# Kernel optimization log

Hardware: AMD Instinct MI355X
Metric: run time of the kernel (lower is better)

## Reference

```python
import jax, jax.numpy as jnp
import numpy as np

SEQ_LEN = 1024
D_MODEL = 512
K_FILT = 24
HEADS = 8
R = 512  # must equal d_model for the module's forward to type-check
NFFT = 2048  # nearest power of two >= 2*SEQ_LEN-1
LN_EPS = 1e-5


def _spectral_filters():
    # Hankel matrix Z[i,j] = 2 / ((i+j)^3 - (i+j)), i,j in 1..T
    e = np.arange(1, SEQ_LEN + 1, dtype=np.float64)
    ipj = e[:, None] + e[None, :]
    Z = 2.0 / (ipj ** 3 - ipj)
    sigma, phi = np.linalg.eigh(Z)
    sigma_k = np.clip(sigma[-K_FILT:], 1e-9, None)
    phi_k = phi[:, -K_FILT:] * sigma_k ** 0.25
    return phi_k.astype(np.float32)  # (T, K)


def setup_inputs() -> dict:
    key = jax.random.key(0)
    ks = jax.random.split(key, 12)
    s = 0.02
    B = 2

    def lin(k):
        kw, kb = jax.random.split(k)
        return (jax.random.normal(kw, (D_MODEL, D_MODEL), jnp.float32) * s,
                jax.random.normal(kb, (D_MODEL,), jnp.float32) * s)

    Wq, bq = lin(ks[0]); Wk, bk = lin(ks[1]); Wv, bv = lin(ks[2])
    Wg, bg = lin(ks[3]); Wo, bo = lin(ks[4])
    return {
        'x': jax.random.normal(ks[5], (B, SEQ_LEN, D_MODEL), jnp.float32),
        'stu_filters': jnp.asarray(_spectral_filters()),
        'M_inputs': jax.random.normal(ks[6], (D_MODEL, R), jnp.float32) * s,
        'M_filters': jax.random.normal(ks[7], (K_FILT, R), jnp.float32) * s,
        'Wq': Wq, 'bq': bq, 'Wk': Wk, 'bk': bk, 'Wv': Wv, 'bv': bv,
        'Wg': Wg, 'bg': bg, 'Wo': Wo, 'bo': bo,
        'ln_w': jnp.ones((R,), jnp.float32),
        'ln_b': jnp.zeros((R,), jnp.float32),
    }


def _stu_conv(u, v):
    # u: (B, T, r), v: (T, r). FFT-based causal conv with sign featurization.
    T = u.shape[1]
    sgn = jnp.where(jnp.arange(T) % 2 == 1, -1.0, 1.0)[None, :, None]  # (1,T,1)
    Vf = jnp.fft.rfft(v[None, :, :, None], n=NFFT, axis=1)  # (1,F,r,1)
    U = jnp.stack([u, u * sgn], axis=-1)  # (B,T,r,2)
    Uf = jnp.fft.rfft(U, n=NFFT, axis=1)  # (B,F,r,2)
    conv = jnp.fft.irfft(Vf * Uf, n=NFFT, axis=1)[:, :T]  # (B,T,r,2)
    return conv[..., 0], conv[..., 1] * sgn


def _layernorm(x, w, b):
    mu = jnp.mean(x, axis=-1, keepdims=True)
    var = jnp.mean((x - mu) ** 2, axis=-1, keepdims=True)
    return (x - mu) * jax.lax.rsqrt(var + LN_EPS) * w + b


def reference(x, stu_filters, M_inputs, M_filters, Wq, bq, Wk, bk, Wv, bv,
              Wg, bg, Wo, bo, ln_w, ln_b):
    B, T, d = x.shape
    hd = d // HEADS
    # STU features
    u_proj = x @ M_inputs                    # (B,T,r)
    phi_proj = stu_filters @ M_filters       # (T,r)
    sp, sm = _stu_conv(u_proj, phi_proj)
    x_tilde = _layernorm(sp + sm, ln_w, ln_b)  # (B,T,r==d)
    # gated linear attention with gelu features and causal cumsum state
    def proj(W, b):
        y = (x @ W.T + b).reshape(B, T, HEADS, hd).transpose(0, 2, 1, 3)
        return jax.nn.gelu(y, approximate=True)
    Q = proj(Wq, bq); K = proj(Wk, bk); V = proj(Wv, bv)
    Zt = jnp.einsum('bhtp,bhtn->bhtpn', V, K)   # (B,H,T,hd,hd)
    Hc = jnp.cumsum(Zt, axis=2)
    Y = jnp.einsum('bhtp,bhtpn->bhtn', Q, Hc)   # (B,H,T,hd)
    Y_attn = Y.transpose(0, 2, 1, 3).reshape(B, T, d)
    gate = jax.nn.sigmoid(x @ Wg.T + bg)
    comb = gate * Y_attn + (1.0 - gate) * x_tilde
    return comb @ Wo.T + bo
```

## Files before the change

### kernel.cpp

```cpp
#include <hip/hip_runtime.h>
#include <hip/hip_bf16.h>

#define T_SEQ 1024
#define D_MOD 512
#define NHEAD 8
#define HDIM  64
#define R_DIM 512
#define BATCH 2

typedef __attribute__((ext_vector_type(8))) __bf16 bf16x8;
typedef __attribute__((ext_vector_type(4))) __bf16 bf16x4;
typedef __attribute__((ext_vector_type(4))) float f32x4;

__device__ __forceinline__ float ldin(const void* p, size_t i, int bf) {
    if (bf) return __bfloat162float(((const __hip_bfloat16*)p)[i]);
    return ((const float*)p)[i];
}
__device__ __forceinline__ void stout(void* p, size_t i, int bf, float v) {
    if (bf) ((__hip_bfloat16*)p)[i] = __float2bfloat16(v);
    else    ((float*)p)[i] = v;
}

__device__ __forceinline__ float gelu_f(float x) {
    return 0.5f * x * (1.f + tanhf(0.7978845608028654f * (x + 0.044715f * x * x * x)));
}

__device__ __forceinline__ bf16x8 cvt8(float4 a, float4 b) {
    bf16x8 t;
    t[0]=(__bf16)a.x; t[1]=(__bf16)a.y; t[2]=(__bf16)a.z; t[3]=(__bf16)a.w;
    t[4]=(__bf16)b.x; t[5]=(__bf16)b.y; t[6]=(__bf16)b.z; t[7]=(__bf16)b.w;
    return t;
}

template<int BF>
__global__ __launch_bounds__(256) void mega_gemm(
    const void* __restrict__ x, const void* __restrict__ Mi,
    const void* __restrict__ stf, const void* __restrict__ Mf,
    const void* __restrict__ Wq, const void* __restrict__ bq,
    const void* __restrict__ Wk, const void* __restrict__ bk,
    const void* __restrict__ Wv, const void* __restrict__ bv,
    const void* __restrict__ Wg, const void* __restrict__ bg,
    __bf16* __restrict__ fu, __bf16* __restrict__ fphi,
    __bf16* __restrict__ fQ, __bf16* __restrict__ fKT,
    __bf16* __restrict__ fV, __bf16* __restrict__ fG)
{
    const int tid = threadIdx.x;
    const int job = blockIdx.z;
    if (job == 6) {
        float4* zp = (float4*)(fphi + 524288);
        const int bid = blockIdx.y * 8 + blockIdx.x;
        const float4 z4 = make_float4(0.f, 0.f, 0.f, 0.f);
        #pragma unroll
        for (int q = 0; q < 8; ++q)
            zp[(size_t)bid * 2048 + q * 256 + tid] = z4;
        return;
    }
    constexpr int bf = BF;
    const void* A = x; const void* Bw; const void* bias = nullptr;
    int Kd = 512, act = 0; bool trb = true;
    switch (job) {
        case 0: Bw = Mi; trb = false; break;
        case 1: Bw = Wq; bias = bq; act = 1; break;
        case 2: Bw = Wk; bias = bk; act = 1; break;
        case 3: Bw = Wv; bias = bv; act = 1; break;
        case 4: Bw = Wg; bias = bg; act = 2; break;
        default: A = stf; Bw = Mf; trb = false; Kd = 32; break;
    }
    const int M = (job == 5) ? 1024 : 2048;
    const int m0 = blockIdx.y * 64;
    if (m0 >= M) return;
    const int n0 = blockIdx.x * 64;

    __shared__ __align__(16) __bf16 As[64][40];
    __shared__ __align__(16) __bf16 Bs[64][40];
    const int wave = tid >> 6, lane = tid & 63;
    const int lm = lane & 15, kq = lane >> 4;

    f32x4 acc[4] = {};

    for (int k0 = 0; k0 < Kd; k0 += 32) {
        if (k0) __syncthreads();
        {
            const int mo = tid >> 2;
            const int ko = (tid & 3) * 8;
            if (job == 5) {
                bf16x8 t;
                #pragma unroll
                for (int q = 0; q < 8; ++q) {
                    const int k = ko + q;
                    t[q] = (k < 24) ? (__bf16)ldin(A, (size_t)(m0 + mo) * 24 + k, bf)
                                    : (__bf16)0.f;
                }
                *(bf16x8*)&As[mo][ko] = t;
            } else if (bf) {
                *(bf16x8*)&As[mo][ko] =
                    *(const bf16x8*)((const __bf16*)A + (size_t)(m0 + mo) * 512 + k0 + ko);
            } else {
                const float* Af = (const float*)A + (size_t)(m0 + mo) * 512 + k0 + ko;
                *(bf16x8*)&As[mo][ko] = cvt8(*(const float4*)Af, *(const float4*)(Af + 4));
            }
        }
        if (trb) {
            const int no = tid >> 2;
            const int ko = (tid & 3) * 8;
            const int cs = ((((ko >> 3) ^ (no >> 3)) & 3) << 3);
            const size_t go = (size_t)(n0 + no) * 512 + k0 + ko;
            if (bf) {
                *(bf16x8*)&Bs[no][cs] = *(const bf16x8*)((const __bf16*)Bw + go);
            } else {
                const float* Bf = (const float*)Bw + go;
                *(bf16x8*)&Bs[no][cs] = cvt8(*(const float4*)Bf, *(const float4*)(Bf + 4));
            }
        } else {
            const int kk = tid >> 3;
            const int nn = (tid & 7) * 8;
            if (job == 5) {
                #pragma unroll
                for (int q = 0; q < 8; ++q) {
                    const int row = nn + q;
                    const int c = ((((kk >> 3) ^ (row >> 3)) & 3) << 3) | (kk & 7);
                    Bs[row][c] = (kk < 24) ? (__bf16)ldin(Bw, (size_t)kk * 512 + n0 + row, bf)
                                           : (__bf16)0.f;
                }
            } else {
                const size_t off = (size_t)(k0 + kk) * 512 + n0 + nn;
                bf16x8 t;
                if (bf) {
                    t = *(const bf16x8*)((const __bf16*)Bw + off);
                } else {
                    const float* Bf = (const float*)Bw + off;
                    t = cvt8(*(const float4*)Bf, *(const float4*)(Bf + 4));
                }
                #pragma unroll
                for (int q = 0; q < 8; ++q) {
                    const int row = nn + q;
                    const int c = ((((kk >> 3) ^ (row >> 3)) & 3) << 3) | (kk & 7);
                    Bs[row][c] = t[q];
                }
            }
        }
        __syncthreads();
        const bf16x8 a = *(const bf16x8*)&As[wave * 16 + lm][kq * 8];
        #pragma unroll
        for (int nt = 0; nt < 4; ++nt) {
            const int row = nt * 16 + lm;
            const bf16x8 b = *(const bf16x8*)&Bs[row][(((kq ^ (row >> 3)) & 3) << 3)];
            acc[nt] = __builtin_amdgcn_mfma_f32_16x16x32_bf16(a, b, acc[nt], 0, 0, 0);
        }
    }
    #pragma unroll
    for (int nt = 0; nt < 4; ++nt) {
        const int n = n0 + nt * 16 + lm;
        #pragma unroll
        for (int r2 = 0; r2 < 4; ++r2) {
            const int m = m0 + wave * 16 + kq * 4 + r2;
            float v = acc[nt][r2];
            if (bias) v += ldin(bias, (size_t)n, bf);
            if (act == 1) v = gelu_f(v);
            if (act == 2) v = 1.f / (1.f + expf(-v));
            switch (job) {
                case 0: fu[(size_t)m * 512 + n] = (__bf16)v; break;
                case 5: fphi[(size_t)m * 512 + n] = (__bf16)v; break;
                case 1: fQ[(size_t)m * 512 + n] = (__bf16)v; break;
                case 3: fV[(size_t)m * 512 + n] = (__bf16)v; break;
                case 4: fG[(size_t)m * 512 + n] = (__bf16)v; break;
                case 2: {
                    const int b = m >> 10, t = m & 1023;
                    const int h = n >> 6,  p = n & 63;
                    fKT[(((size_t)b * NHEAD + h) * 64 + p) * T_SEQ + t] = (__bf16)v;
                    break;
                }
            }
        }
    }
}

__global__ __launch_bounds__(256) void conv_attn_k(
    const __bf16* __restrict__ u, const __bf16* __restrict__ vphi,
    float* __restrict__ w,
    const __bf16* __restrict__ Q, const __bf16* __restrict__ KT,
    const __bf16* __restrict__ V, float* __restrict__ Y)
{
    __shared__ __align__(16) unsigned char smem[49152];
    const int tid = threadIdx.x;
    const int z = blockIdx.z;
    int rem = blockIdx.x, ti = 0;
    while (rem >= ((ti + 4) >> 2)) { rem -= (ti + 4) >> 2; ++ti; }
    const int jlo = rem * 4;
    const int jhi = (jlo + 3 < ti) ? jlo + 3 : ti;
    const int t0 = ti * 64;

    if (z < 2) {
        float (*vs)[64] = (float (*)[64])smem;
        float (*us)[64] = (float (*)[64])(smem + 16384);
        const int rl = tid & 63, tg = tid >> 6;
        const int b = z;
        const int r0 = blockIdx.y * 64;
        const __bf16* ub = u + (size_t)b * T_SEQ * R_DIM;
        float acc[16] = {};
        for (int j = jlo; j <= jhi; ++j) {
            if (j != jlo) __syncthreads();
            const int L0 = j * 64;
            const int W0 = t0 - L0 - 63;
            #pragma unroll
            for (int jj = 0; jj < 8; ++jj) {
                const int n = jj * 256 + tid;
                const int row = n >> 4, c4 = (n & 15) * 4;
                int s = W0 + row;
                s = s < 0 ? 0 : (s > T_SEQ - 1 ? T_SEQ - 1 : s);
                const bf16x4 t = *(const bf16x4*)&ub[(size_t)s * R_DIM + r0 + c4];
                *(float4*)&us[row][c4] =
                    make_float4((float)t[0], (float)t[1], (float)t[2], (float)t[3]);
            }
            #pragma unroll
            for (int jj = 0; jj < 4; ++jj) {
                const int n = jj * 256 + tid;
                const int row = n >> 4, c4 = (n & 15) * 4;
                const bf16x4 t = *(const bf16x4*)&vphi[(size_t)(L0 + row) * R_DIM + r0 + c4];
                *(float4*)&vs[row][c4] =
                    make_float4((float)t[0], (float)t[1], (float)t[2], (float)t[3]);
            }
            __syncthreads();
            if (j < ti) {
                #pragma unroll
                for (int g = 0; g < 4; ++g) {
                    const int wsmin = tg * 16 + 49 - 16 * g;
                    float ur[30];
                    #pragma unroll
                    for (int q = 0; q < 30; ++q) ur[q] = us[wsmin + q][rl];
                    float vr[8];
                    #pragma unroll
                    for (int e = 0; e < 8; ++e) vr[e] = vs[16 * g + 2 * e][rl];
                    #pragma unroll
                    for (int e = 0; e < 8; ++e)
                        #pragma unroll
                        for (int i = 0; i < 16; ++i)
                            acc[i] += vr[e] * ur[i - 2 * e + 14];
                }
            } else {
                for (int l = 0; l < 64; l += 2) {
                    const float vv = vs[l][rl];
                    #pragma unroll
                    for (int i = 0; i < 16; ++i) {
                        const int srel = tg * 16 + i - l;
                        if (srel >= 0) acc[i] += vv * us[srel + 63][rl];
                    }
                }
            }
        }
        #pragma unroll
        for (int i = 0; i < 16; ++i)
            atomicAdd(&w[((size_t)b * T_SEQ + t0 + tg * 16 + i) * R_DIM + r0 + rl],
                      2.f * acc[i]);
    } else {
        __bf16 (*Qs)[72] = (__bf16 (*)[72])smem;
        __bf16 (*Vs)[72] = (__bf16 (*)[72])(smem + 9216);
        __bf16 (*Kt)[72] = (__bf16 (*)[72])(smem + 18432);
        __bf16 (*Sa)[72] = (__bf16 (*)[72])(smem + 27648);
        const int wave = tid >> 6, lane = tid & 63;
        const int lm = lane & 15, kq = lane >> 4;
        const int b = z - 2;
        const int h = blockIdx.y;
        const size_t cbase = ((size_t)b * T_SEQ) * D_MOD + h * HDIM;
        const __bf16* KTh = KT + (((size_t)b * NHEAD + h) * 64) * T_SEQ;
        #pragma unroll
        for (int it = 0; it < 2; ++it) {
            const int n = it * 256 + tid;
            const int row = n >> 3, p0 = (n & 7) * 8;
            *(bf16x8*)&Qs[row][p0] = *(const bf16x8*)&Q[cbase + (size_t)(t0 + row) * D_MOD + p0];
        }
        f32x4 accY[4] = {};
        for (int j = jlo; j <= jhi; ++j) {
            const int s0 = j * 64;
            __syncthreads();
            #pragma unroll
            for (int it = 0; it < 2; ++it) {
                const int n = it * 256 + tid;
                const int row = n >> 3, c0 = (n & 7) * 8;
                *(bf16x8*)&Vs[row][c0] = *(const bf16x8*)&V[cbase + (size_t)(s0 + row) * D_MOD + c0];
                *(bf16x8*)&Kt[row][c0] = *(const bf16x8*)&KTh[(size_t)row * T_SEQ + s0 + c0];
            }
            __syncthreads();
            f32x4 sacc[4] = {};
            #pragma unroll
            for (int ks = 0; ks < 2; ++ks) {
                const bf16x8 a = *(const bf16x8*)&Qs[wave * 16 + lm][ks * 32 + kq * 8];
                #pragma unroll
                for (int nt = 0; nt < 4; ++nt) {
                    const bf16x8 bb = *(const bf16x8*)&Vs[nt * 16 + lm][ks * 32 + kq * 8];
                    sacc[nt] = __builtin_amdgcn_mfma_f32_16x16x32_bf16(a, bb, sacc[nt], 0, 0, 0);
                }
            }
            const bool diag = (j == ti);
            #pragma unroll
            for (int nt = 0; nt < 4; ++nt) {
                const int sl = nt * 16 + lm;
                #pragma unroll
                for (int r2 = 0; r2 < 4; ++r2) {
                    const int tl = wave * 16 + kq * 4 + r2;
                    float v = sacc[nt][r2];
                    if (diag && sl > tl) v = 0.f;
                    Sa[tl][sl] = (__bf16)v;
                }
            }
            #pragma unroll
            for (int ks = 0; ks < 2; ++ks) {
                const bf16x8 a = *(const bf16x8*)&Sa[wave * 16 + lm][ks * 32 + kq * 8];
                #pragma unroll
                for (int nt = 0; nt < 4; ++nt) {
                    const bf16x8 bb = *(const bf16x8*)&Kt[nt * 16 + lm][ks * 32 + kq * 8];
                    accY[nt] = __builtin_amdgcn_mfma_f32_16x16x32_bf16(a, bb, accY[nt], 0, 0, 0);
                }
            }
        }
        #pragma unroll
        for (int nt = 0; nt < 4; ++nt) {
            const int nh = nt * 16 + lm;
            #pragma unroll
            for (int r2 = 0; r2 < 4; ++r2) {
                const int tl = wave * 16 + kq * 4 + r2;
                atomicAdd(&Y[cbase + (size_t)(t0 + tl) * D_MOD + nh], accY[nt][r2]);
            }
        }
    }
}

template<int BF>
__global__ __launch_bounds__(256) void ln_k(const float* __restrict__ w,
                                            __bf16* __restrict__ xt,
                                            const void* __restrict__ g,
                                            const void* __restrict__ b)
{
    constexpr int bf = BF;
    const size_t row = (size_t)blockIdx.y * T_SEQ + blockIdx.x;
    const float* p = w + row * R_DIM;
    const int tid = threadIdx.x;
    const float x0 = p[tid], x1 = p[tid + 256];
    __shared__ float red[4];
    float s = x0 + x1;
    #pragma unroll
    for (int off = 32; off > 0; off >>= 1) s += __shfl_down(s, off, 64);
    if ((tid & 63) == 0) red[tid >> 6] = s;
    __syncthreads();
    const float mu = (red[0] + red[1] + red[2] + red[3]) * (1.f / 512.f);
    __syncthreads();
    const float d0 = x0 - mu, d1 = x1 - mu;
    float vsum = d0 * d0 + d1 * d1;
    #pragma unroll
    for (int off = 32; off > 0; off >>= 1) vsum += __shfl_down(vsum, off, 64);
    if ((tid & 63) == 0) red[tid >> 6] = vsum;
    __syncthreads();
    const float var = (red[0] + red[1] + red[2] + red[3]) * (1.f / 512.f);
    const float rs = rsqrtf(var + 1e-5f);
    __bf16* q = xt + row * R_DIM;
    q[tid]       = (__bf16)(d0 * rs * ldin(g, tid, bf)       + ldin(b, tid, bf));
    q[tid + 256] = (__bf16)(d1 * rs * ldin(g, tid + 256, bf) + ldin(b, tid + 256, bf));
}

template<int BF>
__global__ __launch_bounds__(256) void final_gemm(const __bf16* __restrict__ G,
                                                  const float* __restrict__ Yf,
                                                  const __bf16* __restrict__ Xt,
                                                  const void* __restrict__ Wo,
                                                  const void* __restrict__ bo,
                                                  void* __restrict__ out)
{
    constexpr int bf = BF;
    __shared__ __align__(16) __bf16 sm[2][2 * 64 * 40];
    const int tid = threadIdx.x;
    const int wave = tid >> 6, lane = tid & 63;
    const int lm = lane & 15, kq = lane >> 4;
    const int mo = tid >> 2, ko = (tid & 3) * 8;
    const int m0 = blockIdx.y * 64, n0 = blockIdx.x * 64;

    bf16x8 pg, px, pw;
    float4 py0, py1, pw0, pw1;

    auto issue = [&](int k0) {
        const size_t off = (size_t)(m0 + mo) * 512 + k0 + ko;
        pg  = *(const bf16x8*)(G + off);
        px  = *(const bf16x8*)(Xt + off);
        py0 = *(const float4*)(Yf + off); py1 = *(const float4*)(Yf + off + 4);
        const size_t ob = (size_t)(n0 + mo) * 512 + k0 + ko;
        if (bf) pw = *(const bf16x8*)((const __bf16*)Wo + ob);
        else { const float* Bf = (const float*)Wo + ob;
               pw0 = *(const float4*)Bf; pw1 = *(const float4*)(Bf + 4); }
    };
    auto commit = [&](int bi) {
        __bf16 (*As)[40] = (__bf16 (*)[40])sm[bi];
        __bf16 (*Bs)[40] = (__bf16 (*)[40])(sm[bi] + 64 * 40);
        const float yv[8] = {py0.x,py0.y,py0.z,py0.w,py1.x,py1.y,py1.z,py1.w};
        bf16x8 t;
        #pragma unroll
        for (int q = 0; q < 8; ++q) {
            const float gg = (float)pg[q];
            t[q] = (__bf16)(gg * yv[q] + (1.f - gg) * (float)px[q]);
        }
        *(bf16x8*)&As[mo][ko] = t;
        *(bf16x8*)&Bs[mo][ko] = bf ? pw : cvt8(pw0, pw1);
    };

    f32x4 acc[4] = {};
    issue(0);
    commit(0);
    __syncthreads();
    int cur = 0;
    for (int k0 = 0; k0 < 512; k0 += 32) {
        const bool haveNext = (k0 + 32 < 512);
        if (haveNext) issue(k0 + 32);
        __bf16 (*As)[40] = (__bf16 (*)[40])sm[cur];
        __bf16 (*Bs)[40] = (__bf16 (*)[40])(sm[cur] + 64 * 40);
        const bf16x8 a = *(const bf16x8*)&As[wave * 16 + lm][kq * 8];
        #pragma unroll
        for (int nt = 0; nt < 4; ++nt) {
            const bf16x8 b = *(const bf16x8*)&Bs[nt * 16 + lm][kq * 8];
            acc[nt] = __builtin_amdgcn_mfma_f32_16x16x32_bf16(a, b, acc[nt], 0, 0, 0);
        }
        if (haveNext) {
            commit(cur ^ 1);
            __syncthreads();
            cur ^= 1;
        }
    }
    #pragma unroll
    for (int nt = 0; nt < 4; ++nt) {
        const int n = n0 + nt * 16 + lm;
        #pragma unroll
        for (int r2 = 0; r2 < 4; ++r2) {
            const int m = m0 + wave * 16 + kq * 4 + r2;
            float v = acc[nt][r2] + ldin(bo, (size_t)n, bf);
            stout(out, (size_t)m * 512 + n, bf, v);
        }
    }
}

extern "C" void kernel_launch(void* const* d_in, const int* in_sizes, int n_in,
                              void* d_out, int out_size, void* d_ws, size_t ws_size,
                              hipStream_t stream)
{
    const void* x   = d_in[0];
    const void* stf = d_in[1];
    const void* Mi  = d_in[2];
    const void* Mf  = d_in[3];
    const void* Wq  = d_in[4];  const void* bq = d_in[5];
    const void* Wk  = d_in[6];  const void* bk = d_in[7];
    const void* Wv  = d_in[8];  const void* bv = d_in[9];
    const void* Wg  = d_in[10]; const void* bg = d_in[11];
    const void* Wo  = d_in[12]; const void* bo = d_in[13];
    const void* lnw = d_in[14]; const void* lnb = d_in[15];

    float* base = (float*)d_ws;
    __bf16* f_u   = (__bf16*)base;
    __bf16* f_phi = f_u + 1048576;
    float*  f_w   = base + 786432;
    float*  f_Y   = base + 1835008;
    __bf16* f_xt  = (__bf16*)(base + 2883584);
    __bf16* f_Q   = (__bf16*)(base + 3407872);
    __bf16* f_KT  = f_Q + 1048576;
    __bf16* f_V   = f_KT + 1048576;
    __bf16* f_G   = f_V + 1048576;

    const int bf = (in_sizes[0] == BATCH * T_SEQ * D_MOD * 2);

    dim3 blk(256);

    if (bf)
        mega_gemm<1><<<dim3(8, 32, 7), blk, 0, stream>>>(
            x, Mi, stf, Mf, Wq, bq, Wk, bk, Wv, bv, Wg, bg,
            f_u, f_phi, f_Q, f_KT, f_V, f_G);
    else
        mega_gemm<0><<<dim3(8, 32, 7), blk, 0, stream>>>(
            x, Mi, stf, Mf, Wq, bq, Wk, bk, Wv, bv, Wg, bg,
            f_u, f_phi, f_Q, f_KT, f_V, f_G);

    conv_attn_k<<<dim3(40, 8, 4), blk, 0, stream>>>(f_u, f_phi, f_w, f_Q, f_KT, f_V, f_Y);

    if (bf) ln_k<1><<<dim3(T_SEQ, BATCH), blk, 0, stream>>>(f_w, f_xt, lnw, lnb);
    else    ln_k<0><<<dim3(T_SEQ, BATCH), blk, 0, stream>>>(f_w, f_xt, lnw, lnb);

    if (bf) final_gemm<1><<<dim3(8, 32), blk, 0, stream>>>(f_G, f_Y, f_xt, Wo, bo, d_out);
    else    final_gemm<0><<<dim3(8, 32), blk, 0, stream>>>(f_G, f_Y, f_xt, Wo, bo, d_out);
}
```

Before: 163.5 us.

## Fuse layernorm into final GEMM and double-buffer mega_gemm K loop

Removes the separate layernorm kernel. Each final_gemm block now computes per-row mean and inverse std from the fp32 conv output and applies the normalisation while staging its A tile. Separately, the main projection GEMM now prefetches the next K slice into registers and alternates between two shared-memory buffers, which halves the barriers per step. The fusion makes every column block redundantly recompute the row statistics (8x re-reads of the fp32 rows) and uses a single-pass variance formula, which is numerically less robust.

```diff
diff --git a/kernel.cpp b/kernel.cpp
--- a/kernel.cpp
+++ b/kernel.cpp
@@ -57,95 +57,113 @@
     }
     constexpr int bf = BF;
     const void* A = x; const void* Bw; const void* bias = nullptr;
-    int Kd = 512, act = 0; bool trb = true;
+    int act = 0; bool trb = true;
     switch (job) {
         case 0: Bw = Mi; trb = false; break;
         case 1: Bw = Wq; bias = bq; act = 1; break;
         case 2: Bw = Wk; bias = bk; act = 1; break;
         case 3: Bw = Wv; bias = bv; act = 1; break;
         case 4: Bw = Wg; bias = bg; act = 2; break;
-        default: A = stf; Bw = Mf; trb = false; Kd = 32; break;
+        default: A = stf; Bw = Mf; trb = false; break;
     }
     const int M = (job == 5) ? 1024 : 2048;
     const int m0 = blockIdx.y * 64;
     if (m0 >= M) return;
     const int n0 = blockIdx.x * 64;
 
-    __shared__ __align__(16) __bf16 As[64][40];
-    __shared__ __align__(16) __bf16 Bs[64][40];
+    __shared__ __align__(16) __bf16 As[2][64][40];
+    __shared__ __align__(16) __bf16 Bs[2][64][40];
     const int wave = tid >> 6, lane = tid & 63;
     const int lm = lane & 15, kq = lane >> 4;
+    const int mo = tid >> 2, ko = (tid & 3) * 8;
+    const int kk = tid >> 3, nn = (tid & 7) * 8;
 
     f32x4 acc[4] = {};
 
-    for (int k0 = 0; k0 < Kd; k0 += 32) {
-        if (k0) __syncthreads();
+    if (job == 5) {
         {
-            const int mo = tid >> 2;
-            const int ko = (tid & 3) * 8;
-            if (job == 5) {
-                bf16x8 t;
-                #pragma unroll
-                for (int q = 0; q < 8; ++q) {
-                    const int k = ko + q;
-                    t[q] = (k < 24) ? (__bf16)ldin(A, (size_t)(m0 + mo) * 24 + k, bf)
-                                    : (__bf16)0.f;
-                }
-                *(bf16x8*)&As[mo][ko] = t;
-            } else if (bf) {
-                *(bf16x8*)&As[mo][ko] =
-                    *(const bf16x8*)((const __bf16*)A + (size_t)(m0 + mo) * 512 + k0 + ko);
+            bf16x8 t;
+            #pragma unroll
+            for (int q = 0; q < 8; ++q) {
+                const int k = ko + q;
+                t[q] = (k < 24) ? (__bf16)ldin(A, (size_t)(m0 + mo) * 24 + k, bf)
+                                : (__bf16)0.f;
+            }
+            *(bf16x8*)&As[0][mo][ko] = t;
+        }
+        #pragma unroll
+        for (int q = 0; q < 8; ++q) {
+            const int row = nn + q;
+            const int c = ((((kk >> 3) ^ (row >> 3)) & 3) << 3) | (kk & 7);
+            Bs[0][row][c] = (kk < 24) ? (__bf16)ldin(Bw, (size_t)kk * 512 + n0 + row, bf)
+                                      : (__bf16)0.f;
+        }
+        __syncthreads();
+        const bf16x8 a = *(const bf16x8*)&As[0][wave * 16 + lm][kq * 8];
+        #pragma unroll
+        for (int nt = 0; nt < 4; ++nt) {
+            const int row = nt * 16 + lm;
+            const bf16x8 b = *(const bf16x8*)&Bs[0][row][(((kq ^ (row >> 3)) & 3) << 3)];
+            acc[nt] = __builtin_amdgcn_mfma_f32_16x16x32_bf16(a, b, acc[nt], 0, 0, 0);
+        }
+    } else {
+        bf16x8 rA, rB;
+        float4 a0, a1, b0, b1;
+
+        auto issue = [&](int k0) {
+            if (bf) {
+                rA = *(const bf16x8*)((const __bf16*)A + (size_t)(m0 + mo) * 512 + k0 + ko);
             } else {
                 const float* Af = (const float*)A + (size_t)(m0 + mo) * 512 + k0 + ko;
-                *(bf16x8*)&As[mo][ko] = cvt8(*(const float4*)Af, *(const float4*)(Af + 4));
-            }
-        }
-        if (trb) {
-            const int no = tid >> 2;
-            const int ko = (tid & 3) * 8;
-            const int cs = ((((ko >> 3) ^ (no >> 3)) & 3) << 3);
-            const size_t go = (size_t)(n0 + no) * 512 + k0 + ko;
-            if (bf) {
-                *(bf16x8*)&Bs[no][cs] = *(const bf16x8*)((const __bf16*)Bw + go);
+                a0 = *(const float4*)Af; a1 = *(const float4*)(Af + 4);
+            }
+            if (trb) {
+                const size_t go = (size_t)(n0 + mo) * 512 + k0 + ko;
+                if (bf) rB = *(const bf16x8*)((const __bf16*)Bw + go);
+                else { const float* Bf = (const float*)Bw + go;
+                       b0 = *(const float4*)Bf; b1 = *(const float4*)(Bf + 4); }
             } else {
-                const float* Bf = (const float*)Bw + go;
-                *(bf16x8*)&Bs[no][cs] = cvt8(*(const float4*)Bf, *(const float4*)(Bf + 4));
-            }
-        } else {
-            const int kk = tid >> 3;
-            const int nn = (tid & 7) * 8;
-            if (job == 5) {
+                const size_t off = (size_t)(k0 + kk) * 512 + n0 + nn;
+                if (bf) rB = *(const bf16x8*)((const __bf16*)Bw + off);
+                else { const float* Bf = (const float*)Bw + off;
+                       b0 = *(const float4*)Bf; b1 = *(const float4*)(Bf + 4); }
+            }
+        };
+        auto commit = [&](int bi) {
+            *(bf16x8*)&As[bi][mo][ko] = bf ? rA : cvt8(a0, a1);
+            if (trb) {
+                const int cs = ((((ko >> 3) ^ (mo >> 3)) & 3) << 3);
+                *(bf16x8*)&Bs[bi][mo][cs] = bf ? rB : cvt8(b0, b1);
+            } else {
+                const bf16x8 t = bf ? rB : cvt8(b0, b1);
                 #pragma unroll
                 for (int q = 0; q < 8; ++q) {
                     const int row = nn + q;
                     const int c = ((((kk >> 3) ^ (row >> 3)) & 3) << 3) | (kk & 7);
-                    Bs[row][c] = (kk < 24) ? (__bf16)ldin(Bw, (size_t)kk * 512 + n0 + row, bf)
-                                           : (__bf16)0.f;
-                }
-            } else {
-                const size_t off = (size_t)(k0 + kk) * 512 + n0 + nn;
-                bf16x8 t;
-                if (bf) {
-                    t = *(const bf16x8*)((const __bf16*)Bw + off);
-                } else {
-                    const float* Bf = (const float*)Bw + off;
-                    t = cvt8(*(const float4*)Bf, *(const float4*)(Bf + 4));
-                }
-                #pragma unroll
-                for (int q = 0; q < 8; ++q) {
-                    const int row = nn + q;
-                    const int c = ((((kk >> 3) ^ (row >> 3)) & 3) << 3) | (kk & 7);
-                    Bs[row][c] = t[q];
-                }
-            }
-        }
+                    Bs[bi][row][c] = t[q];
+                }
+            }
+        };
+
+        issue(0);
+        commit(0);
         __syncthreads();
-        const bf16x8 a = *(const bf16x8*)&As[wave * 16 + lm][kq * 8];
-        #pragma unroll
-        for (int nt = 0; nt < 4; ++nt) {
-            const int row = nt * 16 + lm;
-            const bf16x8 b = *(const bf16x8*)&Bs[row][(((kq ^ (row >> 3)) & 3) << 3)];
-            acc[nt] = __builtin_amdgcn_mfma_f32_16x16x32_bf16(a, b, acc[nt], 0, 0, 0);
+        int cur = 0;
+        for (int k0 = 0; k0 < 512; k0 += 32) {
+            const bool hn = (k0 + 32 < 512);
+            if (hn) issue(k0 + 32);
+            const bf16x8 a = *(const bf16x8*)&As[cur][wave * 16 + lm][kq * 8];
+            #pragma unroll
+            for (int nt = 0; nt < 4; ++nt) {
+                const int row = nt * 16 + lm;
+                const bf16x8 b = *(const bf16x8*)&Bs[cur][row][(((kq ^ (row >> 3)) & 3) << 3)];
+                acc[nt] = __builtin_amdgcn_mfma_f32_16x16x32_bf16(a, b, acc[nt], 0, 0, 0);
+            }
+            if (hn) {
+                commit(cur ^ 1);
+                __syncthreads();
+                cur ^= 1;
+            }
         }
     }
     #pragma unroll
@@ -326,75 +344,90 @@
 }
 
 template<int BF>
-__global__ __launch_bounds__(256) void ln_k(const float* __restrict__ w,
-                                            __bf16* __restrict__ xt,
-                                            const void* __restrict__ g,
-                                            const void* __restrict__ b)
-{
-    constexpr int bf = BF;
-    const size_t row = (size_t)blockIdx.y * T_SEQ + blockIdx.x;
-    const float* p = w + row * R_DIM;
-    const int tid = threadIdx.x;
-    const float x0 = p[tid], x1 = p[tid + 256];
-    __shared__ float red[4];
-    float s = x0 + x1;
-    #pragma unroll
-    for (int off = 32; off > 0; off >>= 1) s += __shfl_down(s, off, 64);
-    if ((tid & 63) == 0) red[tid >> 6] = s;
-    __syncthreads();
-    const float mu = (red[0] + red[1] + red[2] + red[3]) * (1.f / 512.f);
-    __syncthreads();
-    const float d0 = x0 - mu, d1 = x1 - mu;
-    float vsum = d0 * d0 + d1 * d1;
-    #pragma unroll
-    for (int off = 32; off > 0; off >>= 1) vsum += __shfl_down(vsum, off, 64);
-    if ((tid & 63) == 0) red[tid >> 6] = vsum;
-    __syncthreads();
-    const float var = (red[0] + red[1] + red[2] + red[3]) * (1.f / 512.f);
-    const float rs = rsqrtf(var + 1e-5f);
-    __bf16* q = xt + row * R_DIM;
-    q[tid]       = (__bf16)(d0 * rs * ldin(g, tid, bf)       + ldin(b, tid, bf));
-    q[tid + 256] = (__bf16)(d1 * rs * ldin(g, tid + 256, bf) + ldin(b, tid + 256, bf));
-}
-
-template<int BF>
 __global__ __launch_bounds__(256) void final_gemm(const __bf16* __restrict__ G,
                                                   const float* __restrict__ Yf,
-                                                  const __bf16* __restrict__ Xt,
+                                                  const float* __restrict__ Wf,
+                                                  const void* __restrict__ lnw,
+                                                  const void* __restrict__ lnb,
                                                   const void* __restrict__ Wo,
                                                   const void* __restrict__ bo,
                                                   void* __restrict__ out)
 {
     constexpr int bf = BF;
     __shared__ __align__(16) __bf16 sm[2][2 * 64 * 40];
+    __shared__ float smu[64], srs[64];
     const int tid = threadIdx.x;
     const int wave = tid >> 6, lane = tid & 63;
     const int lm = lane & 15, kq = lane >> 4;
     const int mo = tid >> 2, ko = (tid & 3) * 8;
     const int m0 = blockIdx.y * 64, n0 = blockIdx.x * 64;
 
-    bf16x8 pg, px, pw;
-    float4 py0, py1, pw0, pw1;
+    {
+        const int r = tid >> 2, q4 = (tid & 3) * 4;
+        const float* wr = Wf + (size_t)(m0 + r) * 512;
+        float s = 0.f, ss = 0.f;
+        #pragma unroll
+        for (int c = 0; c < 32; ++c) {
+            const float4 v = *(const float4*)(wr + q4 + c * 16);
+            s  += v.x + v.y + v.z + v.w;
+            ss += v.x * v.x + v.y * v.y + v.z * v.z + v.w * v.w;
+        }
+        s  += __shfl_xor(s, 1, 64);  s  += __shfl_xor(s, 2, 64);
+        ss += __shfl_xor(ss, 1, 64); ss += __shfl_xor(ss, 2, 64);
+        if ((tid & 3) == 0) {
+            const float mu = s * (1.f / 512.f);
+            float var = ss * (1.f / 512.f) - mu * mu;
+            var = var < 0.f ? 0.f : var;
+            smu[r] = mu;
+            srs[r] = rsqrtf(var + 1e-5f);
+        }
+    }
+    __syncthreads();
+    const float mu = smu[mo], rs = srs[mo];
+
+    bf16x8 pg, pw, pLg, pLb;
+    float4 py0, py1, pv0, pv1, pw0, pw1, pLg0, pLg1, pLb0, pLb1;
 
     auto issue = [&](int k0) {
         const size_t off = (size_t)(m0 + mo) * 512 + k0 + ko;
         pg  = *(const bf16x8*)(G + off);
-        px  = *(const bf16x8*)(Xt + off);
         py0 = *(const float4*)(Yf + off); py1 = *(const float4*)(Yf + off + 4);
+        pv0 = *(const float4*)(Wf + off); pv1 = *(const float4*)(Wf + off + 4);
         const size_t ob = (size_t)(n0 + mo) * 512 + k0 + ko;
-        if (bf) pw = *(const bf16x8*)((const __bf16*)Wo + ob);
-        else { const float* Bf = (const float*)Wo + ob;
-               pw0 = *(const float4*)Bf; pw1 = *(const float4*)(Bf + 4); }
+        if (bf) {
+            pw  = *(const bf16x8*)((const __bf16*)Wo + ob);
+            pLg = *(const bf16x8*)((const __bf16*)lnw + k0 + ko);
+            pLb = *(const bf16x8*)((const __bf16*)lnb + k0 + ko);
+        } else {
+            const float* Bf = (const float*)Wo + ob;
+            pw0 = *(const float4*)Bf; pw1 = *(const float4*)(Bf + 4);
+            const float* Lg = (const float*)lnw + k0 + ko;
+            pLg0 = *(const float4*)Lg; pLg1 = *(const float4*)(Lg + 4);
+            const float* Lb = (const float*)lnb + k0 + ko;
+            pLb0 = *(const float4*)Lb; pLb1 = *(const float4*)(Lb + 4);
+        }
     };
     auto commit = [&](int bi) {
         __bf16 (*As)[40] = (__bf16 (*)[40])sm[bi];
         __bf16 (*Bs)[40] = (__bf16 (*)[40])(sm[bi] + 64 * 40);
         const float yv[8] = {py0.x,py0.y,py0.z,py0.w,py1.x,py1.y,py1.z,py1.w};
+        const float wv[8] = {pv0.x,pv0.y,pv0.z,pv0.w,pv1.x,pv1.y,pv1.z,pv1.w};
+        float gw[8], gb[8];
+        if (bf) {
+            #pragma unroll
+            for (int q = 0; q < 8; ++q) { gw[q] = (float)pLg[q]; gb[q] = (float)pLb[q]; }
+        } else {
+            gw[0]=pLg0.x; gw[1]=pLg0.y; gw[2]=pLg0.z; gw[3]=pLg0.w;
+            gw[4]=pLg1.x; gw[5]=pLg1.y; gw[6]=pLg1.z; gw[7]=pLg1.w;
+            gb[0]=pLb0.x; gb[1]=pLb0.y; gb[2]=pLb0.z; gb[3]=pLb0.w;
+            gb[4]=pLb1.x; gb[5]=pLb1.y; gb[6]=pLb1.z; gb[7]=pLb1.w;
+        }
         bf16x8 t;
         #pragma unroll
         for (int q = 0; q < 8; ++q) {
+            const float xt = (wv[q] - mu) * rs * gw[q] + gb[q];
             const float gg = (float)pg[q];
-            t[q] = (__bf16)(gg * yv[q] + (1.f - gg) * (float)px[q]);
+            t[q] = (__bf16)(gg * yv[q] + (1.f - gg) * xt);
         }
         *(bf16x8*)&As[mo][ko] = t;
         *(bf16x8*)&Bs[mo][ko] = bf ? pw : cvt8(pw0, pw1);
@@ -454,7 +487,6 @@
     __bf16* f_phi = f_u + 1048576;
     float*  f_w   = base + 786432;
     float*  f_Y   = base + 1835008;
-    __bf16* f_xt  = (__bf16*)(base + 2883584);
     __bf16* f_Q   = (__bf16*)(base + 3407872);
     __bf16* f_KT  = f_Q + 1048576;
     __bf16* f_V   = f_KT + 1048576;
@@ -475,9 +507,6 @@
 
     conv_attn_k<<<dim3(40, 8, 4), blk, 0, stream>>>(f_u, f_phi, f_w, f_Q, f_KT, f_V, f_Y);
 
-    if (bf) ln_k<1><<<dim3(T_SEQ, BATCH), blk, 0, stream>>>(f_w, f_xt, lnw, lnb);
-    else    ln_k<0><<<dim3(T_SEQ, BATCH), blk, 0, stream>>>(f_w, f_xt, lnw, lnb);
-
-    if (bf) final_gemm<1><<<dim3(8, 32), blk, 0, stream>>>(f_G, f_Y, f_xt, Wo, bo, d_out);
-    else    final_gemm<0><<<dim3(8, 32), blk, 0, stream>>>(f_G, f_Y, f_xt, Wo, bo, d_out);
-}
+    if (bf) final_gemm<1><<<dim3(8, 32), blk, 0, stream>>>(f_G, f_Y, f_w, lnw, lnb, Wo, bo, d_out);
+    else    final_gemm<0><<<dim3(8, 32), blk, 0, stream>>>(f_G, f_Y, f_w, lnw, lnb, Wo, bo, d_out);
+}
```

Result: no change. 164.9 us (+0.9%).
